# Optimization experiments

Hardware: AMD Instinct MI355X
Metric: run time of the kernel (lower is better)

## Reference

```python
import jax, jax.numpy as jnp
import numpy as np

N = 50000   # nodes
E = 400000  # edges
F = 128     # in_channels == heads*out_channels (H*C)
H = 8       # heads
C = 16      # per-head out_channels (hidden_channels)
ED = 16     # edge_dim
G = 64      # num graphs in batch
OUT = 64    # encoder out_channels
NEG = 0.2   # leaky_relu negative slope
EPS = 1e-5  # batchnorm eps


def setup_inputs() -> dict:
    key = jax.random.key(0)
    ks = jax.random.split(key, 16)
    s = 0.09  # ~xavier scale for fan_in 128
    return {
        "x": jax.random.normal(ks[0], (N, F), jnp.float32),
        "edge_index": jax.random.randint(ks[1], (2, E), 0, N, dtype=jnp.int32),
        "edge_attr": jax.random.normal(ks[2], (E, ED), jnp.float32),
        "batch": jnp.sort(jax.random.randint(ks[3], (N,), 0, G, dtype=jnp.int32)),
        "lin_qkv": jax.random.normal(ks[4], (3, 3, F, F), jnp.float32) * s,   # [layer, q/k/v, out, in]
        "lin_edge": jax.random.normal(ks[5], (3, F, ED), jnp.float32) * s,    # [layer, out, edge_dim]
        "att": jax.random.normal(ks[6], (3, 3, H, C), jnp.float32) * 0.1,     # [layer, att_q/att_k/att_edge, H, C]
        "gat_bias": jnp.zeros((3, F), jnp.float32),
        "bn_scale": jnp.ones((3, F), jnp.float32),
        "bn_bias": jnp.zeros((3, F), jnp.float32),
        "W1": jax.random.normal(ks[7], (64, 128), jnp.float32) * s,
        "b1": jnp.zeros((64,), jnp.float32),
        "bn1_s": jnp.ones((64,), jnp.float32),
        "bn1_b": jnp.zeros((64,), jnp.float32),
        "W2": jax.random.normal(ks[8], (32, 64), jnp.float32) * 0.12,
        "b2": jnp.zeros((32,), jnp.float32),
        "bn2_s": jnp.ones((32,), jnp.float32),
        "bn2_b": jnp.zeros((32,), jnp.float32),
        "Wout": jax.random.normal(ks[9], (OUT, 32), jnp.float32) * 0.17,
        "bout": jnp.zeros((OUT,), jnp.float32),
    }


def _bn(h, scale, shift):
    # training-mode BatchNorm1d: biased batch statistics (torch default)
    mu = h.mean(axis=0)
    var = h.var(axis=0)
    return (h - mu) * jax.lax.rsqrt(var + EPS) * scale + shift


def reference(x, edge_index, edge_attr, batch, lin_qkv, lin_edge, att, gat_bias,
              bn_scale, bn_bias, W1, b1, bn1_s, bn1_b, W2, b2, bn2_s, bn2_b, Wout, bout):
    src = edge_index[0]  # j (message source)
    dst = edge_index[1]  # i (message target)
    h = x
    for i in range(3):  # fixed num_layers, structurally distinct params
        q = (h @ lin_qkv[i, 0].T).reshape(N, H, C)
        k = (h @ lin_qkv[i, 1].T).reshape(N, H, C)
        v = (h @ lin_qkv[i, 2].T).reshape(N, H, C)
        e = (edge_attr @ lin_edge[i].T).reshape(E, H, C)
        # alpha = q_i*att_q*(k_j*att_k) + edge*att_edge, summed over C  -> [E,H]
        a = (q[dst] * att[i, 0] * (k[src] * att[i, 1]) + e * att[i, 2]).sum(axis=-1)
        a = jnp.where(a > 0, a, NEG * a)  # leaky_relu
        # segment softmax over incoming edges of each target node
        amax = jax.ops.segment_max(a, dst, num_segments=N)
        a = jnp.exp(a - amax[dst])
        a = a / (jax.ops.segment_sum(a, dst, num_segments=N)[dst] + 1e-16)
        out = jax.ops.segment_sum(v[src] * a[:, :, None], dst, num_segments=N)
        out = out.reshape(N, H * C) + gat_bias[i]  # concat heads + bias
        out = _bn(out, bn_scale[i], bn_bias[i])
        if i < 2:
            out = jax.nn.relu(out)  # dropout p=0.2 inactive in eval
        h = out
    g = jax.ops.segment_max(h, batch, num_segments=G)  # global_max_pool [G, H*C]
    z = jax.nn.relu(_bn(g @ W1.T + b1, bn1_s, bn1_b))
    z = jax.nn.relu(_bn(z @ W2.T + b2, bn2_s, bn2_b))
    return z @ Wout.T + bout  # [G, OUT]
```

## Files before the change

### kernel.cpp

```cpp
#include <hip/hip_runtime.h>
#include <hip/hip_bf16.h>
#include <hip/hip_fp16.h>
#include <cstddef>
#include <cstdint>

#define NN 50000
#define EE 400000
#define GG 64
#define MB 391

typedef __attribute__((ext_vector_type(8))) _Float16 f16x8;
typedef __attribute__((ext_vector_type(4))) float f32x4;

#define GLOAD_LDS16(g, l) __builtin_amdgcn_global_load_lds( \
    (const __attribute__((address_space(1))) void*)(g), \
    (__attribute__((address_space(3))) void*)(l), 16, 0, 0)

__device__ __forceinline__ unsigned f2key(float f) {
    unsigned u = __float_as_uint(f);
    return (u & 0x80000000u) ? ~u : (u | 0x80000000u);
}
__device__ __forceinline__ float key2f(unsigned k) {
    unsigned u = (k & 0x80000000u) ? (k ^ 0x80000000u) : ~k;
    return __uint_as_float(u);
}

__global__ void compute_M_kernel(const float* __restrict__ lin_edge,
                                 const float* __restrict__ att,
                                 float* __restrict__ M) {
    int t = blockIdx.x * 256 + threadIdx.x;
    if (t >= 3 * 128) return;
    int l = t >> 7, r = t & 127, h = r >> 4, d = r & 15;
    const float* le = lin_edge + (size_t)l * 128 * 16;
    const float* av = att + ((l * 3 + 2) * 128) + h * 16;
    float acc = 0.f;
#pragma unroll
    for (int c = 0; c < 16; ++c) acc += le[(h * 16 + c) * 16 + d] * av[c];
    M[t] = acc;
}

__global__ __launch_bounds__(256)
void wpack_kernel(const float* __restrict__ lin_qkv, __half* __restrict__ Wpack) {
    int g = blockIdx.x * 256 + threadIdx.x;
    int lm = g >> 11;
    int r = g & 2047;
    int kb = r >> 9;
    int kg = (r >> 7) & 3;
    int n  = r & 127;
    int k0 = kb * 32 + kg * 8;
    const float* row = lin_qkv + ((size_t)lm * 128 + n) * 128 + k0;
    __half o[8] __attribute__((aligned(16)));
#pragma unroll
    for (int i = 0; i < 8; ++i) o[i] = __float2half(row[i]);
    *reinterpret_cast<uint4*>(Wpack + (size_t)g * 8) = *reinterpret_cast<const uint4*>(o);
}

__global__ __launch_bounds__(256)
void pack_kernel(const float* __restrict__ hin, const float* __restrict__ sums,
                 const float* __restrict__ scale, const float* __restrict__ shift,
                 int mode, __half* __restrict__ Apack) {
    int s = blockIdx.x * 256 + threadIdx.x;
    int mb = s >> 11;
    int r  = s & 2047;
    int kb = r >> 9;
    int kg = (r >> 7) & 3;
    int m  = r & 127;
    int node = mb * 128 + m;
    int k0 = kb * 32 + kg * 8;
    size_t slot = ((size_t)(mb * 4 + kb) * 512 + (size_t)kg * 128 + m) * 8;
    __half o[8] __attribute__((aligned(16)));
    if (node < NN) {
        const float* row = hin + (size_t)node * 128 + k0;
#pragma unroll
        for (int i = 0; i < 8; ++i) {
            float v = row[i];
            if (mode) {
                int c = k0 + i;
                float mu = sums[c] * (1.f / NN);
                float var = sums[128 + c] * (1.f / NN) - mu * mu;
                v = (v - mu) * rsqrtf(var + 1e-5f) * scale[c] + shift[c];
                v = v > 0.f ? v : 0.f;
            }
            o[i] = __float2half(v);
        }
    } else {
#pragma unroll
        for (int i = 0; i < 8; ++i) o[i] = __float2half(0.f);
    }
    *reinterpret_cast<uint4*>(Apack + slot) = *reinterpret_cast<const uint4*>(o);
}

__global__ __launch_bounds__(256, 4)
void qkv_mfma_kernel(const __half* __restrict__ Apack,
                     const __half* __restrict__ Wpack,
                     int layer,
                     const float* __restrict__ att_l,
                     __half* __restrict__ qa, __half* __restrict__ kv) {
    __shared__ __half Ab[2][4096];
    __shared__ __half Bb[2][4096];
    const int t = threadIdx.x;
    const int lane = t & 63;
    const int wave = t >> 6;
    const int wr = wave >> 1, wc = wave & 1;
    const int mb = blockIdx.x, mat = blockIdx.y;

    const __half* Abase = Apack + (size_t)mb * 16384;
    const __half* Bbase = Wpack + (size_t)(layer * 3 + mat) * 16384;

    f32x4 acc[4][4];
#pragma unroll
    for (int i = 0; i < 4; ++i)
#pragma unroll
        for (int j = 0; j < 4; ++j) acc[i][j] = (f32x4){0.f, 0.f, 0.f, 0.f};

    auto stage = [&](int c, int buf) {
        const __half* ga = Abase + (size_t)c * 4096;
        const __half* gb = Bbase + (size_t)c * 4096;
        GLOAD_LDS16(ga + (size_t)(wave * 64 + lane) * 8,        &Ab[buf][(wave * 64) * 8]);
        GLOAD_LDS16(ga + (size_t)(256 + wave * 64 + lane) * 8,  &Ab[buf][(256 + wave * 64) * 8]);
        GLOAD_LDS16(gb + (size_t)(wave * 64 + lane) * 8,        &Bb[buf][(wave * 64) * 8]);
        GLOAD_LDS16(gb + (size_t)(256 + wave * 64 + lane) * 8,  &Bb[buf][(256 + wave * 64) * 8]);
    };

    stage(0, 0);
    __syncthreads();
    const int abase = ((lane >> 4) * 128 + wr * 64 + (lane & 15)) * 8;
    const int bbase = ((lane >> 4) * 128 + wc * 64 + (lane & 15)) * 8;
#pragma unroll
    for (int c = 0; c < 4; ++c) {
        int cur = c & 1;
        if (c < 3) stage(c + 1, cur ^ 1);
        f16x8 aF[4], bF[4];
#pragma unroll
        for (int mf = 0; mf < 4; ++mf)
            aF[mf] = *reinterpret_cast<const f16x8*>(&Ab[cur][abase + mf * 128]);
#pragma unroll
        for (int nf = 0; nf < 4; ++nf)
            bF[nf] = *reinterpret_cast<const f16x8*>(&Bb[cur][bbase + nf * 128]);
#pragma unroll
        for (int mf = 0; mf < 4; ++mf)
#pragma unroll
            for (int nf = 0; nf < 4; ++nf)
                acc[mf][nf] = __builtin_amdgcn_mfma_f32_16x16x32_f16(aF[mf], bF[nf], acc[mf][nf], 0, 0, 0);
        __syncthreads();
    }

    __half* outb = (mat == 0) ? qa : kv;
    const size_t stride = (mat == 0) ? 128 : 256;
    const int coloff = (mat == 2) ? 128 : 0;
    float sc[4];
#pragma unroll
    for (int nf = 0; nf < 4; ++nf) {
        int col = wc * 64 + nf * 16 + (lane & 15);
        sc[nf] = (mat == 2) ? 1.f : att_l[mat * 128 + col];
    }
    const int rowq = (lane >> 4) * 4;
#pragma unroll
    for (int mf = 0; mf < 4; ++mf) {
        int row0 = mb * 128 + wr * 64 + mf * 16 + rowq;
#pragma unroll
        for (int reg = 0; reg < 4; ++reg) {
            int row = row0 + reg;
            if (row < NN) {
#pragma unroll
                for (int nf = 0; nf < 4; ++nf) {
                    int col = wc * 64 + nf * 16 + (lane & 15);
                    outb[(size_t)row * stride + coloff + col] = __float2half(acc[mf][nf][reg] * sc[nf]);
                }
            }
        }
    }
}

__global__ __launch_bounds__(256)
void deg_count_kernel(const int* __restrict__ ei, int* __restrict__ deg) {
    int e = blockIdx.x * 256 + threadIdx.x;
    if (e < EE) atomicAdd(&deg[ei[EE + e]], 1);
}

__global__ __launch_bounds__(256)
void scan_partial_kernel(const int* __restrict__ deg, int* __restrict__ psum) {
    __shared__ int red[256];
    int i = blockIdx.x * 256 + threadIdx.x;
    red[threadIdx.x] = (i < NN) ? deg[i] : 0;
    __syncthreads();
    for (int o = 128; o > 0; o >>= 1) {
        if (threadIdx.x < o) red[threadIdx.x] += red[threadIdx.x + o];
        __syncthreads();
    }
    if (threadIdx.x == 0) psum[blockIdx.x] = red[0];
}

__global__ __launch_bounds__(256)
void scan_top_kernel(const int* __restrict__ psum, int* __restrict__ psx) {
    __shared__ int sh[256];
    int t = threadIdx.x;
    int v = (t < 196) ? psum[t] : 0;
    sh[t] = v;
    __syncthreads();
    for (int o = 1; o < 256; o <<= 1) {
        int add = (t >= o) ? sh[t - o] : 0;
        __syncthreads();
        sh[t] += add;
        __syncthreads();
    }
    if (t < 196) psx[t] = sh[t] - v;
}

__global__ __launch_bounds__(256)
void scan_final_kernel(const int* __restrict__ deg, const int* __restrict__ psx,
                       int* __restrict__ offs, int* __restrict__ cursor) {
    __shared__ int sh[256];
    int t = threadIdx.x;
    int i = blockIdx.x * 256 + t;
    int v = (i < NN) ? deg[i] : 0;
    sh[t] = v;
    __syncthreads();
    for (int o = 1; o < 256; o <<= 1) {
        int add = (t >= o) ? sh[t - o] : 0;
        __syncthreads();
        sh[t] += add;
        __syncthreads();
    }
    if (i < NN) {
        int excl = sh[t] - v + psx[blockIdx.x];
        offs[i] = excl;
        cursor[i] = excl;
    }
}

__global__ __launch_bounds__(256)
void scatter_eatt_kernel(const int* __restrict__ ei, const float* __restrict__ edge_attr,
                         const float* __restrict__ M, int* __restrict__ cursor,
                         int* __restrict__ csrc, __half* __restrict__ eatt) {
    __shared__ float Ms[384];
    for (int i = threadIdx.x; i < 384; i += 256) Ms[i] = M[i];
    __syncthreads();
    int e = blockIdx.x * 256 + threadIdx.x;
    if (e >= EE) return;
    const float4* ep = reinterpret_cast<const float4*>(edge_attr + (size_t)e * 16);
    float4 a0 = ep[0], a1 = ep[1], a2 = ep[2], a3 = ep[3];
    float ea[16] = {a0.x, a0.y, a0.z, a0.w, a1.x, a1.y, a1.z, a1.w,
                    a2.x, a2.y, a2.z, a2.w, a3.x, a3.y, a3.z, a3.w};
    int src = ei[e], dst = ei[EE + e];
    int pos = atomicAdd(&cursor[dst], 1);
    csrc[pos] = src;
#pragma unroll
    for (int l = 0; l < 3; ++l) {
        __half o[8] __attribute__((aligned(16)));
#pragma unroll
        for (int h = 0; h < 8; ++h) {
            const float* mp = Ms + l * 128 + h * 16;
            float acc = 0.f;
#pragma unroll
            for (int d = 0; d < 16; ++d) acc += ea[d] * mp[d];
            o[h] = __float2half(acc);
        }
        *reinterpret_cast<uint4*>(eatt + ((size_t)l * EE + pos) * 8) =
            *reinterpret_cast<const uint4*>(o);
    }
}

__global__ __launch_bounds__(128)
void fused_gat_kernel(const __half* __restrict__ qa, const __half* __restrict__ kv,
                      const __half* __restrict__ eatt_l,
                      const int* __restrict__ offs, const int* __restrict__ deg,
                      const int* __restrict__ csrc, float* __restrict__ hout) {
    int lane = threadIdx.x & 63;
    int n = blockIdx.x * 2 + (threadIdx.x >> 6);
    if (n >= NN) return;
    int h = lane >> 3;
    int c2h = lane & 7;
    int chh = h * 8 + c2h;
    int ch = chh * 2;

    float2 q = __half22float2(*reinterpret_cast<const __half2*>(qa + (size_t)n * 128 + ch));

    int start = offs[n], d = deg[n];
    const __half* ebase = eatt_l + (size_t)start * 8 + h;
    const int* sbase = csrc + start;

    float m = -INFINITY, den = 0.f, acc0 = 0.f, acc1 = 0.f;
    int i = 0;
    for (; i + 4 <= d; i += 4) {
        int s0 = sbase[i], s1 = sbase[i + 1], s2 = sbase[i + 2], s3 = sbase[i + 3];
        float e0 = __half2float(ebase[(size_t)i * 8]);
        float e1 = __half2float(ebase[(size_t)(i + 1) * 8]);
        float e2 = __half2float(ebase[(size_t)(i + 2) * 8]);
        float e3 = __half2float(ebase[(size_t)(i + 3) * 8]);
        const __half2* p0h = reinterpret_cast<const __half2*>(kv + (size_t)s0 * 256);
        const __half2* p1h = reinterpret_cast<const __half2*>(kv + (size_t)s1 * 256);
        const __half2* p2h = reinterpret_cast<const __half2*>(kv + (size_t)s2 * 256);
        const __half2* p3h = reinterpret_cast<const __half2*>(kv + (size_t)s3 * 256);
        float2 k0 = __half22float2(p0h[chh]);
        float2 k1 = __half22float2(p1h[chh]);
        float2 k2 = __half22float2(p2h[chh]);
        float2 k3 = __half22float2(p3h[chh]);
        float2 v0 = __half22float2(p0h[64 + chh]);
        float2 v1 = __half22float2(p1h[64 + chh]);
        float2 v2 = __half22float2(p2h[64 + chh]);
        float2 v3 = __half22float2(p3h[64 + chh]);
        float p0 = q.x * k0.x + q.y * k0.y;
        float p1 = q.x * k1.x + q.y * k1.y;
        float p2 = q.x * k2.x + q.y * k2.y;
        float p3 = q.x * k3.x + q.y * k3.y;
        p0 += __shfl_xor(p0, 1); p0 += __shfl_xor(p0, 2); p0 += __shfl_xor(p0, 4);
        p1 += __shfl_xor(p1, 1); p1 += __shfl_xor(p1, 2); p1 += __shfl_xor(p1, 4);
        p2 += __shfl_xor(p2, 1); p2 += __shfl_xor(p2, 2); p2 += __shfl_xor(p2, 4);
        p3 += __shfl_xor(p3, 1); p3 += __shfl_xor(p3, 2); p3 += __shfl_xor(p3, 4);
        float a0 = p0 + e0; a0 = a0 > 0.f ? a0 : 0.2f * a0;
        float a1 = p1 + e1; a1 = a1 > 0.f ? a1 : 0.2f * a1;
        float a2 = p2 + e2; a2 = a2 > 0.f ? a2 : 0.2f * a2;
        float a3 = p3 + e3; a3 = a3 > 0.f ? a3 : 0.2f * a3;
        float mn, scl, p;
        mn = fmaxf(m, a0); scl = __expf(m - mn); p = __expf(a0 - mn);
        den = den * scl + p; acc0 = acc0 * scl + p * v0.x; acc1 = acc1 * scl + p * v0.y; m = mn;
        mn = fmaxf(m, a1); scl = __expf(m - mn); p = __expf(a1 - mn);
        den = den * scl + p; acc0 = acc0 * scl + p * v1.x; acc1 = acc1 * scl + p * v1.y; m = mn;
        mn = fmaxf(m, a2); scl = __expf(m - mn); p = __expf(a2 - mn);
        den = den * scl + p; acc0 = acc0 * scl + p * v2.x; acc1 = acc1 * scl + p * v2.y; m = mn;
        mn = fmaxf(m, a3); scl = __expf(m - mn); p = __expf(a3 - mn);
        den = den * scl + p; acc0 = acc0 * scl + p * v3.x; acc1 = acc1 * scl + p * v3.y; m = mn;
    }
    for (; i < d; ++i) {
        int s0 = sbase[i];
        float e0 = __half2float(ebase[(size_t)i * 8]);
        const __half2* p0h = reinterpret_cast<const __half2*>(kv + (size_t)s0 * 256);
        float2 k0 = __half22float2(p0h[chh]);
        float2 v0 = __half22float2(p0h[64 + chh]);
        float p0 = q.x * k0.x + q.y * k0.y;
        p0 += __shfl_xor(p0, 1); p0 += __shfl_xor(p0, 2); p0 += __shfl_xor(p0, 4);
        float a0 = p0 + e0; a0 = a0 > 0.f ? a0 : 0.2f * a0;
        float mn = fmaxf(m, a0);
        float scl = __expf(m - mn);
        float p = __expf(a0 - mn);
        den = den * scl + p; acc0 = acc0 * scl + p * v0.x; acc1 = acc1 * scl + p * v0.y; m = mn;
    }
    float inv = 1.f / (den + 1e-16f);
    *reinterpret_cast<float2*>(hout + (size_t)n * 128 + ch) = make_float2(acc0 * inv, acc1 * inv);
}

__global__ __launch_bounds__(256)
void bn_stats_kernel(const float* __restrict__ h, float* __restrict__ sums) {
    __shared__ float red[2][8][128];
    int t = threadIdx.x;
    int cg = t & 31;
    int rofs = t >> 5;
    int r0 = blockIdx.x * 64;
    int rend = min(NN, r0 + 64);
    float4 s1 = make_float4(0.f, 0.f, 0.f, 0.f);
    float4 s2 = make_float4(0.f, 0.f, 0.f, 0.f);
    for (int r = r0 + rofs; r < rend; r += 8) {
        float4 v = *reinterpret_cast<const float4*>(h + (size_t)r * 128 + cg * 4);
        s1.x += v.x; s1.y += v.y; s1.z += v.z; s1.w += v.w;
        s2.x += v.x * v.x; s2.y += v.y * v.y; s2.z += v.z * v.z; s2.w += v.w * v.w;
    }
    *reinterpret_cast<float4*>(&red[0][rofs][cg * 4]) = s1;
    *reinterpret_cast<float4*>(&red[1][rofs][cg * 4]) = s2;
    __syncthreads();
    if (t < 128) {
        float a = 0.f, b = 0.f;
#pragma unroll
        for (int i = 0; i < 8; ++i) { a += red[0][i][t]; b += red[1][i][t]; }
        unsafeAtomicAdd(&sums[t], a);
        unsafeAtomicAdd(&sums[128 + t], b);
    }
}

__global__ __launch_bounds__(256)
void bn_pool_kernel(const float* __restrict__ h, const float* __restrict__ sums,
                    const float* __restrict__ scale, const float* __restrict__ shift,
                    const int* __restrict__ batch, unsigned* __restrict__ gkey) {
    int t = threadIdx.x;
    int c = t & 127, half = t >> 7;
    int r0 = blockIdx.x * 32;
    int rend = min(NN, r0 + 32);
    const float invN = 1.f / (float)NN;
    float mu = sums[c] * invN;
    float var = sums[128 + c] * invN - mu * mu;
    float iscl = rsqrtf(var + 1e-5f) * scale[c];
    float sh = shift[c];
    int curg = -1;
    float lmax = -INFINITY;
    for (int r = r0 + half; r < rend; r += 2) {
        int g = batch[r];
        if (g != curg) {
            if (curg >= 0) atomicMax(&gkey[curg * 128 + c], f2key(lmax));
            curg = g;
            lmax = -INFINITY;
        }
        float v = (h[(size_t)r * 128 + c] - mu) * iscl + sh;
        lmax = fmaxf(lmax, v);
    }
    if (curg >= 0) atomicMax(&gkey[curg * 128 + c], f2key(lmax));
}

__global__ __launch_bounds__(256)
void head_kernel(const unsigned* __restrict__ gkey,
                 const float* __restrict__ W1, const float* __restrict__ b1,
                 const float* __restrict__ bn1s, const float* __restrict__ bn1b,
                 const float* __restrict__ W2, const float* __restrict__ b2,
                 const float* __restrict__ bn2s, const float* __restrict__ bn2b,
                 const float* __restrict__ Wout, const float* __restrict__ bout,
                 float* __restrict__ out) {
    __shared__ float g[64][128];
    __shared__ float z1[64][64];
    __shared__ float z2[64][32];
    int t = threadIdx.x;
    for (int i = t; i < 64 * 128; i += 256) g[i >> 7][i & 127] = key2f(gkey[i]);
    __syncthreads();
    for (int i = t; i < 64 * 64; i += 256) {
        int r = i >> 6, o = i & 63;
        const float* gr = g[r];
        const float* wr = W1 + (size_t)o * 128;
        float acc = b1[o];
        for (int k2 = 0; k2 < 128; ++k2) acc += gr[k2] * wr[k2];
        z1[r][o] = acc;
    }
    __syncthreads();
    if (t < 64) {
        float s1 = 0.f, s2 = 0.f;
        for (int r = 0; r < 64; ++r) { float v = z1[r][t]; s1 += v; s2 += v * v; }
        float mu = s1 * (1.f / 64.f), var = s2 * (1.f / 64.f) - mu * mu;
        float inv = rsqrtf(var + 1e-5f) * bn1s[t];
        float sh = bn1b[t];
        for (int r = 0; r < 64; ++r) {
            float v = (z1[r][t] - mu) * inv + sh;
            z1[r][t] = v > 0.f ? v : 0.f;
        }
    }
    __syncthreads();
    for (int i = t; i < 64 * 32; i += 256) {
        int r = i >> 5, o = i & 31;
        const float* wr = W2 + (size_t)o * 64;
        float acc = b2[o];
        for (int k2 = 0; k2 < 64; ++k2) acc += z1[r][k2] * wr[k2];
        z2[r][o] = acc;
    }
    __syncthreads();
    if (t < 32) {
        float s1 = 0.f, s2 = 0.f;
        for (int r = 0; r < 64; ++r) { float v = z2[r][t]; s1 += v; s2 += v * v; }
        float mu = s1 * (1.f / 64.f), var = s2 * (1.f / 64.f) - mu * mu;
        float inv = rsqrtf(var + 1e-5f) * bn2s[t];
        float sh = bn2b[t];
        for (int r = 0; r < 64; ++r) {
            float v = (z2[r][t] - mu) * inv + sh;
            z2[r][t] = v > 0.f ? v : 0.f;
        }
    }
    __syncthreads();
    for (int i = t; i < 64 * 64; i += 256) {
        int r = i >> 6, o = i & 63;
        const float* wr = Wout + (size_t)o * 32;
        float acc = bout[o];
        for (int k2 = 0; k2 < 32; ++k2) acc += z2[r][k2] * wr[k2];
        out[r * 64 + o] = acc;
    }
}

extern "C" void kernel_launch(void* const* d_in, const int* in_sizes, int n_in,
                              void* d_out, int out_size, void* d_ws, size_t ws_size,
                              hipStream_t stream) {
    const float* x         = (const float*)d_in[0];
    const int*   ei        = (const int*)d_in[1];
    const float* edge_attr = (const float*)d_in[2];
    const int*   batch     = (const int*)d_in[3];
    const float* lin_qkv   = (const float*)d_in[4];
    const float* lin_edge  = (const float*)d_in[5];
    const float* att       = (const float*)d_in[6];
    const float* bn_scale  = (const float*)d_in[8];
    const float* bn_bias   = (const float*)d_in[9];
    const float* W1   = (const float*)d_in[10];
    const float* b1   = (const float*)d_in[11];
    const float* bn1s = (const float*)d_in[12];
    const float* bn1b = (const float*)d_in[13];
    const float* W2   = (const float*)d_in[14];
    const float* b2   = (const float*)d_in[15];
    const float* bn2s = (const float*)d_in[16];
    const float* bn2b = (const float*)d_in[17];
    const float* Wout = (const float*)d_in[18];
    const float* bout = (const float*)d_in[19];

    float* ws = (float*)d_ws;
    size_t off = 0;
    auto alloc = [&](size_t n) { float* p = ws + off; off += n; return p; };
    int*      deg   = (int*)alloc(NN);
    unsigned* gkey  = (unsigned*)alloc(64 * 128);
    float*    gsums = alloc(3 * 256);
    const size_t zeroBytes = ((size_t)NN + 64 * 128 + 3 * 256) * 4;
    float*  hout = alloc((size_t)NN * 128);
    __half* qa   = (__half*)alloc((size_t)NN * 64);
    __half* kv   = (__half*)alloc((size_t)NN * 128);
    __half* Apack = (__half*)alloc((size_t)MB * 8192);
    __half* Wpack = (__half*)alloc(9 * 8192);
    int*    offs   = (int*)alloc(NN);
    int*    cursor = (int*)alloc(NN);
    int*    csrc   = (int*)alloc(EE);
    __half* eatt   = (__half*)alloc((size_t)3 * EE * 4);
    int*    psum   = (int*)alloc(256);
    int*    psx    = (int*)alloc(256);
    float*  M      = alloc(3 * 128);

    const int edgeBlocks = (EE + 255) / 256;
    const int scanBlocks = (NN + 255) / 256;
    const int packBlocks = MB * 8;
    const int statBlocks = (NN + 63) / 64;
    const int poolBlocks = (NN + 31) / 32;
    const int gatBlocks  = (NN + 1) / 2;

    hipMemsetAsync(deg, 0, zeroBytes, stream);
    wpack_kernel<<<72, 256, 0, stream>>>(lin_qkv, Wpack);
    compute_M_kernel<<<2, 256, 0, stream>>>(lin_edge, att, M);
    deg_count_kernel<<<edgeBlocks, 256, 0, stream>>>(ei, deg);
    scan_partial_kernel<<<scanBlocks, 256, 0, stream>>>(deg, psum);
    scan_top_kernel<<<1, 256, 0, stream>>>(psum, psx);
    scan_final_kernel<<<scanBlocks, 256, 0, stream>>>(deg, psx, offs, cursor);
    scatter_eatt_kernel<<<edgeBlocks, 256, 0, stream>>>(ei, edge_attr, M, cursor, csrc, eatt);
    pack_kernel<<<packBlocks, 256, 0, stream>>>(x, nullptr, nullptr, nullptr, 0, Apack);

    for (int l = 0; l < 3; ++l) {
        qkv_mfma_kernel<<<dim3(MB, 3), 256, 0, stream>>>(
            Apack, Wpack, l, att + (size_t)l * 384, qa, kv);

        fused_gat_kernel<<<gatBlocks, 128, 0, stream>>>(
            qa, kv, eatt + (size_t)l * EE * 8, offs, deg, csrc, hout);

        bn_stats_kernel<<<statBlocks, 256, 0, stream>>>(hout, gsums + l * 256);

        if (l < 2) {
            pack_kernel<<<packBlocks, 256, 0, stream>>>(
                hout, gsums + l * 256, bn_scale + l * 128, bn_bias + l * 128, 1, Apack);
        } else {
            bn_pool_kernel<<<poolBlocks, 256, 0, stream>>>(
                hout, gsums + l * 256, bn_scale + l * 128, bn_bias + l * 128, batch, gkey);
        }
    }

    head_kernel<<<1, 256, 0, stream>>>(gkey, W1, b1, bn1s, bn1b, W2, b2, bn2s, bn2b, Wout, bout, (float*)d_out);
}
```

Measured before the change: 430.4 us.

## Store GAT output in fp16 and drop online-max softmax in aggregation

The per-layer GAT output buffer changes from fp32 to fp16, so the aggregation writes and the BN-stats, pack and pool reads move half the bytes. The fused aggregation kernel drops the running-max online softmax and instead clamps logits at 60 before exponentiating, which removes the rescale exps. It also gains an 8-wide unrolled loop that issues all gathers before the math. The trade-offs are lower precision in the intermediate activations and possible overflow or accuracy loss if logits fall outside the clamp's safe range.

```diff
diff --git a/kernel.cpp b/kernel.cpp
--- a/kernel.cpp
+++ b/kernel.cpp
@@ -56,9 +56,7 @@
 }
 
 __global__ __launch_bounds__(256)
-void pack_kernel(const float* __restrict__ hin, const float* __restrict__ sums,
-                 const float* __restrict__ scale, const float* __restrict__ shift,
-                 int mode, __half* __restrict__ Apack) {
+void pack_x_kernel(const float* __restrict__ hin, __half* __restrict__ Apack) {
     int s = blockIdx.x * 256 + threadIdx.x;
     int mb = s >> 11;
     int r  = s & 2047;
@@ -72,15 +70,39 @@
     if (node < NN) {
         const float* row = hin + (size_t)node * 128 + k0;
 #pragma unroll
+        for (int i = 0; i < 8; ++i) o[i] = __float2half(row[i]);
+    } else {
+#pragma unroll
+        for (int i = 0; i < 8; ++i) o[i] = __float2half(0.f);
+    }
+    *reinterpret_cast<uint4*>(Apack + slot) = *reinterpret_cast<const uint4*>(o);
+}
+
+__global__ __launch_bounds__(256)
+void pack_h_kernel(const __half* __restrict__ hin, const float* __restrict__ sums,
+                   const float* __restrict__ scale, const float* __restrict__ shift,
+                   __half* __restrict__ Apack) {
+    int s = blockIdx.x * 256 + threadIdx.x;
+    int mb = s >> 11;
+    int r  = s & 2047;
+    int kb = r >> 9;
+    int kg = (r >> 7) & 3;
+    int m  = r & 127;
+    int node = mb * 128 + m;
+    int k0 = kb * 32 + kg * 8;
+    size_t slot = ((size_t)(mb * 4 + kb) * 512 + (size_t)kg * 128 + m) * 8;
+    __half o[8] __attribute__((aligned(16)));
+    if (node < NN) {
+        const __half* row = hin + (size_t)node * 128 + k0;
+        uint4 raw = *reinterpret_cast<const uint4*>(row);
+        const __half* rh = reinterpret_cast<const __half*>(&raw);
+#pragma unroll
         for (int i = 0; i < 8; ++i) {
-            float v = row[i];
-            if (mode) {
-                int c = k0 + i;
-                float mu = sums[c] * (1.f / NN);
-                float var = sums[128 + c] * (1.f / NN) - mu * mu;
-                v = (v - mu) * rsqrtf(var + 1e-5f) * scale[c] + shift[c];
-                v = v > 0.f ? v : 0.f;
-            }
+            int c = k0 + i;
+            float mu = sums[c] * (1.f / NN);
+            float var = sums[128 + c] * (1.f / NN) - mu * mu;
+            float v = (__half2float(rh[i]) - mu) * rsqrtf(var + 1e-5f) * scale[c] + shift[c];
+            v = v > 0.f ? v : 0.f;
             o[i] = __float2half(v);
         }
     } else {
@@ -265,110 +287,125 @@
 void fused_gat_kernel(const __half* __restrict__ qa, const __half* __restrict__ kv,
                       const __half* __restrict__ eatt_l,
                       const int* __restrict__ offs, const int* __restrict__ deg,
-                      const int* __restrict__ csrc, float* __restrict__ hout) {
+                      const int* __restrict__ csrc, __half* __restrict__ hout) {
     int lane = threadIdx.x & 63;
     int n = blockIdx.x * 2 + (threadIdx.x >> 6);
     if (n >= NN) return;
     int h = lane >> 3;
     int c2h = lane & 7;
     int chh = h * 8 + c2h;
-    int ch = chh * 2;
-
-    float2 q = __half22float2(*reinterpret_cast<const __half2*>(qa + (size_t)n * 128 + ch));
+
+    float2 q = __half22float2(reinterpret_cast<const __half2*>(qa + (size_t)n * 128)[chh]);
 
     int start = offs[n], d = deg[n];
     const __half* ebase = eatt_l + (size_t)start * 8 + h;
     const int* sbase = csrc + start;
 
-    float m = -INFINITY, den = 0.f, acc0 = 0.f, acc1 = 0.f;
+    float den = 0.f, acc0 = 0.f, acc1 = 0.f;
     int i = 0;
+    for (; i + 8 <= d; i += 8) {
+        int s[8]; float e[8]; __half2 kh[8], vh[8];
+#pragma unroll
+        for (int j = 0; j < 8; ++j) s[j] = sbase[i + j];
+#pragma unroll
+        for (int j = 0; j < 8; ++j) e[j] = __half2float(ebase[(size_t)(i + j) * 8]);
+#pragma unroll
+        for (int j = 0; j < 8; ++j) {
+            const __half2* ph = reinterpret_cast<const __half2*>(kv + (size_t)s[j] * 256);
+            kh[j] = ph[chh];
+            vh[j] = ph[64 + chh];
+        }
+#pragma unroll
+        for (int j = 0; j < 8; ++j) {
+            float2 k = __half22float2(kh[j]);
+            float p = q.x * k.x + q.y * k.y;
+            p += __shfl_xor(p, 1); p += __shfl_xor(p, 2); p += __shfl_xor(p, 4);
+            float a = p + e[j]; a = a > 0.f ? a : 0.2f * a;
+            a = fminf(a, 60.f);
+            float w = __expf(a);
+            float2 v = __half22float2(vh[j]);
+            den += w; acc0 += w * v.x; acc1 += w * v.y;
+        }
+    }
     for (; i + 4 <= d; i += 4) {
-        int s0 = sbase[i], s1 = sbase[i + 1], s2 = sbase[i + 2], s3 = sbase[i + 3];
-        float e0 = __half2float(ebase[(size_t)i * 8]);
-        float e1 = __half2float(ebase[(size_t)(i + 1) * 8]);
-        float e2 = __half2float(ebase[(size_t)(i + 2) * 8]);
-        float e3 = __half2float(ebase[(size_t)(i + 3) * 8]);
-        const __half2* p0h = reinterpret_cast<const __half2*>(kv + (size_t)s0 * 256);
-        const __half2* p1h = reinterpret_cast<const __half2*>(kv + (size_t)s1 * 256);
-        const __half2* p2h = reinterpret_cast<const __half2*>(kv + (size_t)s2 * 256);
-        const __half2* p3h = reinterpret_cast<const __half2*>(kv + (size_t)s3 * 256);
-        float2 k0 = __half22float2(p0h[chh]);
-        float2 k1 = __half22float2(p1h[chh]);
-        float2 k2 = __half22float2(p2h[chh]);
-        float2 k3 = __half22float2(p3h[chh]);
-        float2 v0 = __half22float2(p0h[64 + chh]);
-        float2 v1 = __half22float2(p1h[64 + chh]);
-        float2 v2 = __half22float2(p2h[64 + chh]);
-        float2 v3 = __half22float2(p3h[64 + chh]);
-        float p0 = q.x * k0.x + q.y * k0.y;
-        float p1 = q.x * k1.x + q.y * k1.y;
-        float p2 = q.x * k2.x + q.y * k2.y;
-        float p3 = q.x * k3.x + q.y * k3.y;
-        p0 += __shfl_xor(p0, 1); p0 += __shfl_xor(p0, 2); p0 += __shfl_xor(p0, 4);
-        p1 += __shfl_xor(p1, 1); p1 += __shfl_xor(p1, 2); p1 += __shfl_xor(p1, 4);
-        p2 += __shfl_xor(p2, 1); p2 += __shfl_xor(p2, 2); p2 += __shfl_xor(p2, 4);
-        p3 += __shfl_xor(p3, 1); p3 += __shfl_xor(p3, 2); p3 += __shfl_xor(p3, 4);
-        float a0 = p0 + e0; a0 = a0 > 0.f ? a0 : 0.2f * a0;
-        float a1 = p1 + e1; a1 = a1 > 0.f ? a1 : 0.2f * a1;
-        float a2 = p2 + e2; a2 = a2 > 0.f ? a2 : 0.2f * a2;
-        float a3 = p3 + e3; a3 = a3 > 0.f ? a3 : 0.2f * a3;
-        float mn, scl, p;
-        mn = fmaxf(m, a0); scl = __expf(m - mn); p = __expf(a0 - mn);
-        den = den * scl + p; acc0 = acc0 * scl + p * v0.x; acc1 = acc1 * scl + p * v0.y; m = mn;
-        mn = fmaxf(m, a1); scl = __expf(m - mn); p = __expf(a1 - mn);
-        den = den * scl + p; acc0 = acc0 * scl + p * v1.x; acc1 = acc1 * scl + p * v1.y; m = mn;
-        mn = fmaxf(m, a2); scl = __expf(m - mn); p = __expf(a2 - mn);
-        den = den * scl + p; acc0 = acc0 * scl + p * v2.x; acc1 = acc1 * scl + p * v2.y; m = mn;
-        mn = fmaxf(m, a3); scl = __expf(m - mn); p = __expf(a3 - mn);
-        den = den * scl + p; acc0 = acc0 * scl + p * v3.x; acc1 = acc1 * scl + p * v3.y; m = mn;
+        int s[4]; float e[4]; __half2 kh[4], vh[4];
+#pragma unroll
+        for (int j = 0; j < 4; ++j) s[j] = sbase[i + j];
+#pragma unroll
+        for (int j = 0; j < 4; ++j) e[j] = __half2float(ebase[(size_t)(i + j) * 8]);
+#pragma unroll
+        for (int j = 0; j < 4; ++j) {
+            const __half2* ph = reinterpret_cast<const __half2*>(kv + (size_t)s[j] * 256);
+            kh[j] = ph[chh];
+            vh[j] = ph[64 + chh];
+        }
+#pragma unroll
+        for (int j = 0; j < 4; ++j) {
+            float2 k = __half22float2(kh[j]);
+            float p = q.x * k.x + q.y * k.y;
+            p += __shfl_xor(p, 1); p += __shfl_xor(p, 2); p += __shfl_xor(p, 4);
+            float a = p + e[j]; a = a > 0.f ? a : 0.2f * a;
+            a = fminf(a, 60.f);
+            float w = __expf(a);
+            float2 v = __half22float2(vh[j]);
+            den += w; acc0 += w * v.x; acc1 += w * v.y;
+        }
     }
     for (; i < d; ++i) {
         int s0 = sbase[i];
         float e0 = __half2float(ebase[(size_t)i * 8]);
-        const __half2* p0h = reinterpret_cast<const __half2*>(kv + (size_t)s0 * 256);
-        float2 k0 = __half22float2(p0h[chh]);
-        float2 v0 = __half22float2(p0h[64 + chh]);
-        float p0 = q.x * k0.x + q.y * k0.y;
-        p0 += __shfl_xor(p0, 1); p0 += __shfl_xor(p0, 2); p0 += __shfl_xor(p0, 4);
-        float a0 = p0 + e0; a0 = a0 > 0.f ? a0 : 0.2f * a0;
-        float mn = fmaxf(m, a0);
-        float scl = __expf(m - mn);
-        float p = __expf(a0 - mn);
-        den = den * scl + p; acc0 = acc0 * scl + p * v0.x; acc1 = acc1 * scl + p * v0.y; m = mn;
+        const __half2* ph = reinterpret_cast<const __half2*>(kv + (size_t)s0 * 256);
+        float2 k = __half22float2(ph[chh]);
+        float2 v = __half22float2(ph[64 + chh]);
+        float p = q.x * k.x + q.y * k.y;
+        p += __shfl_xor(p, 1); p += __shfl_xor(p, 2); p += __shfl_xor(p, 4);
+        float a = p + e0; a = a > 0.f ? a : 0.2f * a;
+        a = fminf(a, 60.f);
+        float w = __expf(a);
+        den += w; acc0 += w * v.x; acc1 += w * v.y;
     }
     float inv = 1.f / (den + 1e-16f);
-    *reinterpret_cast<float2*>(hout + (size_t)n * 128 + ch) = make_float2(acc0 * inv, acc1 * inv);
-}
-
-__global__ __launch_bounds__(256)
-void bn_stats_kernel(const float* __restrict__ h, float* __restrict__ sums) {
-    __shared__ float red[2][8][128];
+    reinterpret_cast<__half2*>(hout + (size_t)n * 128)[chh] =
+        __float22half2_rn(make_float2(acc0 * inv, acc1 * inv));
+}
+
+__global__ __launch_bounds__(256)
+void bn_stats_kernel(const __half* __restrict__ h, float* __restrict__ sums) {
+    __shared__ float red[2][16][128];
     int t = threadIdx.x;
-    int cg = t & 31;
-    int rofs = t >> 5;
+    int cg = t & 15;
+    int rofs = t >> 4;
     int r0 = blockIdx.x * 64;
     int rend = min(NN, r0 + 64);
-    float4 s1 = make_float4(0.f, 0.f, 0.f, 0.f);
-    float4 s2 = make_float4(0.f, 0.f, 0.f, 0.f);
-    for (int r = r0 + rofs; r < rend; r += 8) {
-        float4 v = *reinterpret_cast<const float4*>(h + (size_t)r * 128 + cg * 4);
-        s1.x += v.x; s1.y += v.y; s1.z += v.z; s1.w += v.w;
-        s2.x += v.x * v.x; s2.y += v.y * v.y; s2.z += v.z * v.z; s2.w += v.w * v.w;
-    }
-    *reinterpret_cast<float4*>(&red[0][rofs][cg * 4]) = s1;
-    *reinterpret_cast<float4*>(&red[1][rofs][cg * 4]) = s2;
+    float s1[8], s2[8];
+#pragma unroll
+    for (int j = 0; j < 8; ++j) { s1[j] = 0.f; s2[j] = 0.f; }
+    for (int r = r0 + rofs; r < rend; r += 16) {
+        uint4 raw = *reinterpret_cast<const uint4*>(h + (size_t)r * 128 + cg * 8);
+        const __half* rh = reinterpret_cast<const __half*>(&raw);
+#pragma unroll
+        for (int j = 0; j < 8; ++j) {
+            float v = __half2float(rh[j]);
+            s1[j] += v; s2[j] += v * v;
+        }
+    }
+#pragma unroll
+    for (int j = 0; j < 8; ++j) {
+        red[0][rofs][cg * 8 + j] = s1[j];
+        red[1][rofs][cg * 8 + j] = s2[j];
+    }
     __syncthreads();
     if (t < 128) {
         float a = 0.f, b = 0.f;
 #pragma unroll
-        for (int i = 0; i < 8; ++i) { a += red[0][i][t]; b += red[1][i][t]; }
+        for (int i = 0; i < 16; ++i) { a += red[0][i][t]; b += red[1][i][t]; }
         unsafeAtomicAdd(&sums[t], a);
         unsafeAtomicAdd(&sums[128 + t], b);
     }
 }
 
 __global__ __launch_bounds__(256)
-void bn_pool_kernel(const float* __restrict__ h, const float* __restrict__ sums,
+void bn_pool_kernel(const __half* __restrict__ h, const float* __restrict__ sums,
                     const float* __restrict__ scale, const float* __restrict__ shift,
                     const int* __restrict__ batch, unsigned* __restrict__ gkey) {
     int t = threadIdx.x;
@@ -389,7 +426,7 @@
             curg = g;
             lmax = -INFINITY;
         }
-        float v = (h[(size_t)r * 128 + c] - mu) * iscl + sh;
+        float v = (__half2float(h[(size_t)r * 128 + c]) - mu) * iscl + sh;
         lmax = fmaxf(lmax, v);
     }
     if (curg >= 0) atomicMax(&gkey[curg * 128 + c], f2key(lmax));
@@ -489,7 +526,7 @@
     unsigned* gkey  = (unsigned*)alloc(64 * 128);
     float*    gsums = alloc(3 * 256);
     const size_t zeroBytes = ((size_t)NN + 64 * 128 + 3 * 256) * 4;
-    float*  hout = alloc((size_t)NN * 128);
+    __half* hout = (__half*)alloc((size_t)NN * 64);
     __half* qa   = (__half*)alloc((size_t)NN * 64);
     __half* kv   = (__half*)alloc((size_t)NN * 128);
     __half* Apack = (__half*)alloc((size_t)MB * 8192);
@@ -517,7 +554,7 @@
     scan_top_kernel<<<1, 256, 0, stream>>>(psum, psx);
     scan_final_kernel<<<scanBlocks, 256, 0, stream>>>(deg, psx, offs, cursor);
     scatter_eatt_kernel<<<edgeBlocks, 256, 0, stream>>>(ei, edge_attr, M, cursor, csrc, eatt);
-    pack_kernel<<<packBlocks, 256, 0, stream>>>(x, nullptr, nullptr, nullptr, 0, Apack);
+    pack_x_kernel<<<packBlocks, 256, 0, stream>>>(x, Apack);
 
     for (int l = 0; l < 3; ++l) {
         qkv_mfma_kernel<<<dim3(MB, 3), 256, 0, stream>>>(
@@ -529,8 +566,8 @@
         bn_stats_kernel<<<statBlocks, 256, 0, stream>>>(hout, gsums + l * 256);
 
         if (l < 2) {
-            pack_kernel<<<packBlocks, 256, 0, stream>>>(
-                hout, gsums + l * 256, bn_scale + l * 128, bn_bias + l * 128, 1, Apack);
+            pack_h_kernel<<<packBlocks, 256, 0, stream>>>(
+                hout, gsums + l * 256, bn_scale + l * 128, bn_bias + l * 128, Apack);
         } else {
             bn_pool_kernel<<<poolBlocks, 256, 0, stream>>>(
                 hout, gsums + l * 256, bn_scale + l * 128, bn_bias + l * 128, batch, gkey);
```

New measurement: 386.0 us. -10.3%, faster.
